# Performance work log

Hardware: AMD Instinct MI355X
Metric: run time of the kernel (lower is better)

## Reference

```python
import jax, jax.numpy as jnp
import numpy as np

N, S, C, G = 40000, 16, 96, 12
EPS = 1e-5

def ln(x, g, b):
    mu = jnp.mean(x, -1, keepdims=True)
    var = jnp.mean((x - mu) ** 2, -1, keepdims=True)
    return (x - mu) * jax.lax.rsqrt(var + EPS) * g + b

def setup_inputs() -> dict:
    key = jax.random.key(0)
    ks = jax.random.split(key, 20)
    s = 0.05
    inp = {
        'q': jax.random.normal(ks[0], (N, C), jnp.float32),
        'k': jax.random.normal(ks[1], (N, C), jnp.float32),
        'v': jax.random.normal(ks[2], (N, C), jnp.float32),
        'xyz': jax.random.normal(ks[3], (N, 3), jnp.float32),
        'reference_index': jax.random.randint(ks[4], (N, S), 0, N, jnp.int32),
        # linear_q: Linear(C,C)+LN(C)+ReLU
        'Wq': jax.random.normal(ks[5], (C, C), jnp.float32) * s,
        'bq': jnp.zeros((C,), jnp.float32),
        'gq': jnp.ones((C,), jnp.float32),
        'betaq': jnp.zeros((C,), jnp.float32),
        # linear_k
        'Wk': jax.random.normal(ks[6], (C, C), jnp.float32) * s,
        'bk': jnp.zeros((C,), jnp.float32),
        'gk': jnp.ones((C,), jnp.float32),
        'betak': jnp.zeros((C,), jnp.float32),
        # linear_v
        'Wv': jax.random.normal(ks[7], (C, C), jnp.float32) * s,
        'bv': jnp.zeros((C,), jnp.float32),
        # linear_p_bias: Linear(3,C)+LN(C)+ReLU+Linear(C,C)
        'Wp1': jax.random.normal(ks[8], (3, C), jnp.float32) * s,
        'bp1': jnp.zeros((C,), jnp.float32),
        'gp': jnp.ones((C,), jnp.float32),
        'betap': jnp.zeros((C,), jnp.float32),
        'Wp2': jax.random.normal(ks[9], (C, C), jnp.float32) * s,
        'bp2': jnp.zeros((C,), jnp.float32),
        # weight_encoding: Linear(C,G)+LN(G)+ReLU+Linear(G,G)
        'Ww1': jax.random.normal(ks[10], (C, G), jnp.float32) * s,
        'bw1': jnp.zeros((G,), jnp.float32),
        'gw': jnp.ones((G,), jnp.float32),
        'betaw': jnp.zeros((G,), jnp.float32),
        'Ww2': jax.random.normal(ks[11], (G, G), jnp.float32) * s,
        'bw2': jnp.zeros((G,), jnp.float32),
    }
    return inp

def reference(q, k, v, xyz, reference_index,
              Wq, bq, gq, betaq, Wk, bk, gk, betak, Wv, bv,
              Wp1, bp1, gp, betap, Wp2, bp2,
              Ww1, bw1, gw, betaw, Ww2, bw2):
    query = jax.nn.relu(ln(q @ Wq + bq, gq, betaq))            # [N, C]
    keyf  = jax.nn.relu(ln(k @ Wk + bk, gk, betak))            # [N, C]
    val   = v @ Wv + bv                                        # [N, C]

    idx = reference_index                                      # [N, S]
    mask = (idx >= 0).astype(q.dtype)                          # sign(idx+1)
    safe = jnp.clip(idx, 0, None)
    # pointops.grouping: gather w/ zero-fill at idx=-1; with_xyz prepends relative coords
    pos  = (xyz[safe] - xyz[:, None, :]) * mask[..., None]     # [N, S, 3]
    keyg = keyf[safe] * mask[..., None]                        # [N, S, C]
    valg = val[safe] * mask[..., None]                         # [N, S, C]

    rel = keyg - query[:, None, :]                             # [N, S, C]
    peb = jax.nn.relu(ln(pos @ Wp1 + bp1, gp, betap)) @ Wp2 + bp2
    rel = rel + peb
    valg = valg + peb

    w = jax.nn.relu(ln(rel @ Ww1 + bw1, gw, betaw)) @ Ww2 + bw2  # [N, S, G]
    w = jax.nn.softmax(w, axis=1) * mask[..., None]              # softmax over neighbors

    valg = valg.reshape(N, S, G, C // G)
    feat = jnp.einsum('nsgi,nsg->ngi', valg, w).reshape(N, C)
    return feat
```

## Files before the change

kernel.cpp:

```cpp
#include <hip/hip_runtime.h>

#define NN 40000
#define SS 16
#define CC 96
#define GG 12
#define CP 100

typedef __attribute__((ext_vector_type(8))) short bf16x8;
typedef __attribute__((ext_vector_type(4))) float f32x4;

__device__ __forceinline__ short f2bf(float f) {
    union { float f; unsigned u; } c; c.f = f;
    unsigned r = (c.u + 0x7fffu + ((c.u >> 16) & 1u)) >> 16;
    return (short)r;
}
__device__ __forceinline__ unsigned pack2bf(float hi, float lo) {
    unsigned a = __float_as_uint(hi) + 0x8000u;
    unsigned b = __float_as_uint(lo) + 0x8000u;
    return __builtin_amdgcn_perm(a, b, 0x07060302u);
}

template<int CTRL>
__device__ __forceinline__ float dppf(float x) {
    int r = __builtin_amdgcn_mov_dpp(__float_as_int(x), CTRL, 0xF, 0xF, true);
    return __int_as_float(r);
}
__device__ __forceinline__ float row16_sum(float x) {
    x += dppf<0xB1>(x);
    x += dppf<0x4E>(x);
    x += dppf<0x141>(x);
    x += dppf<0x140>(x);
    return x;
}
__device__ __forceinline__ float row16_max(float x) {
    x = fmaxf(x, dppf<0xB1>(x));
    x = fmaxf(x, dppf<0x4E>(x));
    x = fmaxf(x, dppf<0x141>(x));
    x = fmaxf(x, dppf<0x140>(x));
    return x;
}

#define J_W3   27648
#define J_P2   (J_W3 + 9216)
#define J_W1   (J_P2 + 1536)
#define J_WF   (J_W1 + 1536)
#define J_CF   (J_WF + 12)
#define J_S4   (J_CF + 4)
#define J_G    (J_S4 + 16)

__global__ void prep_kernel(const float* __restrict__ Wq, const float* __restrict__ Wk,
                            const float* __restrict__ Wv, const float* __restrict__ Wp2,
                            const float* __restrict__ Ww1, const float* __restrict__ bp2,
                            const float* __restrict__ bw1, const float* __restrict__ Wp1,
                            const float* __restrict__ bp1,
                            ushort* __restrict__ fragQKV, ushort* __restrict__ fragP2,
                            ushort* __restrict__ fragW1, ushort* __restrict__ fragWf,
                            float* __restrict__ cfused, float* __restrict__ stats)
{
    const int job = blockIdx.x*256 + threadIdx.x;
    if (job < J_W3) {
        const int which = job / 9216, o = job % 9216;
        const float* W = (which == 0) ? Wq : (which == 1) ? Wk : Wv;
        const int pos = o >> 3, j = o & 7;
        const int lane = pos & 63, ntkb = pos >> 6;
        const int nt = ntkb / 3, kb = ntkb - nt*3;
        const int col = nt*16 + (lane & 15), krow = kb*32 + (lane >> 4)*8 + j;
        fragQKV[job] = (ushort)f2bf(W[krow*CC + col]);
    } else if (job < J_P2) {
        const int o = job - J_W3;
        const int pos = o >> 3, j = o & 7;
        const int lane = pos & 63, ntkb = pos >> 6;
        const int nt = ntkb / 3, kb = ntkb - nt*3;
        const int col = nt*16 + (lane & 15), krow = kb*32 + (lane >> 4)*8 + j;
        fragP2[o] = (ushort)f2bf(Wp2[krow*CC + col]);
    } else if (job < J_W1) {
        const int o = job - J_P2;
        const int pos = o >> 3, j = o & 7;
        const int lane = pos & 63, kb = pos >> 6;
        const int col = lane & 15, krow = kb*32 + (lane >> 4)*8 + j;
        fragW1[o] = (col < GG) ? (ushort)f2bf(Ww1[krow*GG + col]) : (ushort)0;
    } else if (job < J_WF) {
        const int o = job - J_W1;
        const int pos = o >> 3, j = o & 7;
        const int lane = pos & 63, kb = pos >> 6;
        const int col = lane & 15, krow = kb*32 + (lane >> 4)*8 + j;
        float s = 0.f;
        if (col < GG) for (int jj = 0; jj < CC; ++jj) s += Wp2[krow*CC + jj] * Ww1[jj*GG + col];
        fragWf[o] = (col < GG) ? (ushort)f2bf(s) : (ushort)0;
    } else if (job < J_CF) {
        const int g = job - J_WF;
        float s = bw1[g];
        for (int jj = 0; jj < CC; ++jj) s += bp2[jj] * Ww1[jj*GG + g];
        cfused[g] = s;
    } else if (job < J_S4) {
        const int d = job - J_CF;
        float s = 0.f;
        for (int c = 0; c < CC; ++c) s += (d < 3) ? Wp1[d*CC + c] : bp1[c];
        stats[d] = s;
    } else if (job < J_G) {
        const int o = job - J_S4, d1 = o >> 2, d2 = o & 3;
        float s = 0.f;
        for (int c = 0; c < CC; ++c) {
            const float a1 = (d1 < 3) ? Wp1[d1*CC + c] : bp1[c];
            const float a2 = (d2 < 3) ? Wp1[d2*CC + c] : bp1[c];
            s += a1*a2;
        }
        stats[4 + o] = s;
    }
}

__global__ __launch_bounds__(256) void qkv_mfma(
    const float* __restrict__ q, const float* __restrict__ kx, const float* __restrict__ v,
    const float* __restrict__ bq, const float* __restrict__ gq, const float* __restrict__ betaq,
    const float* __restrict__ bk, const float* __restrict__ gk, const float* __restrict__ betak,
    const float* __restrict__ bv,
    const ushort* __restrict__ fragQKV, const ushort* __restrict__ fragW1,
    float* __restrict__ valout, float* __restrict__ qw1out, float* __restrict__ kw1out)
{
    __shared__ __align__(16) ushort sWf[9216];
    __shared__ float sbias[CC], sg[CC], sbeta[CC];
    __shared__ float sx[4][SS*CP];

    const int p = blockIdx.y;
    const float* X; const float* b;
    const float* g = nullptr; const float* beta = nullptr;
    if (p == 0)      { X = q;  b = bq; g = gq; beta = betaq; }
    else if (p == 1) { X = kx; b = bk; g = gk; beta = betak; }
    else             { X = v;  b = bv; }
    const bool has_ln = (p < 2);
    float* w1out = (p == 0) ? qw1out : kw1out;

    const int t = threadIdx.x;
    if (t < CC) {
        sbias[t] = b[t];
        if (has_ln) { sg[t] = g[t]; sbeta[t] = beta[t]; }
    }
    {
        const uint4* src = (const uint4*)(fragQKV + p*9216);
        for (int i = t; i < 1152; i += 256) ((uint4*)sWf)[i] = src[i];
    }

    const int lane = t & 63, w = t >> 6;
    const int c16 = lane & 15, quad = lane >> 4;

    bf16x8 Ww1f[3];
    if (has_ln) {
        #pragma unroll
        for (int kb = 0; kb < 3; ++kb) {
            union { bf16x8 v; uint4 u; } wu;
            wu.u = ((const uint4*)fragW1)[kb*64 + lane];
            Ww1f[kb] = wu.v;
        }
    }

    __syncthreads();

    const f32x4 zero4 = {0.f, 0.f, 0.f, 0.f};
    float* sxw = sx[w];
    const int tile = blockIdx.x*4 + w;
    const int row0 = tile * 16;

    const float* xr = X + (size_t)(row0 + c16)*CC;
    bf16x8 Af[3];
    #pragma unroll
    for (int kb = 0; kb < 3; ++kb) {
        const float4 a0 = *(const float4*)(xr + kb*32 + quad*8);
        const float4 a1 = *(const float4*)(xr + kb*32 + quad*8 + 4);
        union { bf16x8 v; uint u[4]; } au;
        au.u[0] = pack2bf(a0.y, a0.x);
        au.u[1] = pack2bf(a0.w, a0.z);
        au.u[2] = pack2bf(a1.y, a1.x);
        au.u[3] = pack2bf(a1.w, a1.z);
        Af[kb] = au.v;
    }

    f32x4 acc[6];
    #pragma unroll
    for (int nt = 0; nt < 6; ++nt) acc[nt] = zero4;
    #pragma unroll
    for (int kb = 0; kb < 3; ++kb)
        #pragma unroll
        for (int nt = 0; nt < 6; ++nt) {
            const bf16x8 bf = *(const bf16x8*)(sWf + ((nt*3 + kb)*64 + lane)*8);
            acc[nt] = __builtin_amdgcn_mfma_f32_16x16x32_bf16(Af[kb], bf, acc[nt], 0, 0, 0);
        }

    #pragma unroll
    for (int nt = 0; nt < 6; ++nt) {
        const float bb = sbias[nt*16 + c16];
        #pragma unroll
        for (int r = 0; r < 4; ++r) acc[nt][r] += bb;
    }

    if (has_ln) {
        #pragma unroll
        for (int r = 0; r < 4; ++r) {
            float sum = 0.f, sq = 0.f;
            #pragma unroll
            for (int nt = 0; nt < 6; ++nt) { float x = acc[nt][r]; sum += x; sq += x*x; }
            sum = row16_sum(sum); sq = row16_sum(sq);
            const float mu  = sum * (1.f/96.f);
            const float var = sq * (1.f/96.f) - mu*mu;
            const float rs  = rsqrtf(var + 1e-5f);
            #pragma unroll
            for (int nt = 0; nt < 6; ++nt) {
                const int c = nt*16 + c16;
                acc[nt][r] = fmaxf((acc[nt][r] - mu)*rs*sg[c] + sbeta[c], 0.f);
            }
        }
        #pragma unroll
        for (int nt = 0; nt < 6; ++nt)
            #pragma unroll
            for (int r = 0; r < 4; ++r)
                sxw[(quad*4 + r)*CP + nt*16 + c16] = acc[nt][r];

        bf16x8 aA[3];
        #pragma unroll
        for (int kb = 0; kb < 3; ++kb) {
            const float4 a0 = *(const float4*)(sxw + c16*CP + kb*32 + quad*8);
            const float4 a1 = *(const float4*)(sxw + c16*CP + kb*32 + quad*8 + 4);
            union { bf16x8 v; uint u[4]; } au;
            au.u[0] = pack2bf(a0.y, a0.x);
            au.u[1] = pack2bf(a0.w, a0.z);
            au.u[2] = pack2bf(a1.y, a1.x);
            au.u[3] = pack2bf(a1.w, a1.z);
            aA[kb] = au.v;
        }
        f32x4 o = zero4;
        #pragma unroll
        for (int kb = 0; kb < 3; ++kb)
            o = __builtin_amdgcn_mfma_f32_16x16x32_bf16(aA[kb], Ww1f[kb], o, 0, 0, 0);
        if (c16 < GG) {
            #pragma unroll
            for (int r = 0; r < 4; ++r)
                w1out[(size_t)(row0 + quad*4 + r)*GG + c16] = o[r];
        }
    } else {
        #pragma unroll
        for (int r = 0; r < 4; ++r)
            #pragma unroll
            for (int nt = 0; nt < 6; ++nt)
                valout[(size_t)(row0 + quad*4 + r)*CC + nt*16 + c16] = acc[nt][r];
    }
}

__global__ __launch_bounds__(256) void attn2(
    const float* __restrict__ xyz, const int* __restrict__ refidx,
    const float* __restrict__ gp,  const float* __restrict__ betap,
    const float* __restrict__ Wp1, const float* __restrict__ bp1,
    const float* __restrict__ bp2,
    const float* __restrict__ gw,  const float* __restrict__ betaw,
    const float* __restrict__ Ww2, const float* __restrict__ bw2,
    const float* __restrict__ cfused, const float* __restrict__ stats,
    const ushort* __restrict__ fragP2, const ushort* __restrict__ fragWf,
    const float* __restrict__ valw, const float* __restrict__ kw1w, const float* __restrict__ qw1w,
    float* __restrict__ out)
{
    __shared__ __align__(16) ushort sWp2f[9216];
    __shared__ __align__(16) ushort sWffl[1536];
    __shared__ float4 sA[CC];
    __shared__ float2 sGB[CC];
    __shared__ float  sbp2[CC];
    __shared__ float  sWw2[GG*GG];
    __shared__ float  sgw[16], sbetaw[16], sbw2[16], scf[16];
    __shared__ float  sstats[20];
    __shared__ float  ybv[4][SS*GG];
    __shared__ float  swv[4][SS*GG];

    const int t = threadIdx.x;
    if (t < CC) {
        sA[t]  = make_float4(Wp1[t], Wp1[CC + t], Wp1[2*CC + t], bp1[t]);
        sGB[t] = make_float2(gp[t], betap[t]);
        sbp2[t] = bp2[t];
    }
    if (t < GG*GG) sWw2[t] = Ww2[t];
    if (t < 16) {
        sgw[t]    = (t < GG) ? gw[t]     : 0.f;
        sbetaw[t] = (t < GG) ? betaw[t]  : 0.f;
        sbw2[t]   = (t < GG) ? bw2[t]    : 0.f;
        scf[t]    = (t < GG) ? cfused[t] : 0.f;
    }
    if (t < 20) sstats[t] = stats[t];
    for (int i = t; i < 1152; i += 256) ((uint4*)sWp2f)[i] = ((const uint4*)fragP2)[i];
    if (t < 192) ((uint4*)sWffl)[t] = ((const uint4*)fragWf)[t];

    const int lane = t & 63, w = t >> 6;
    const int c16 = lane & 15, quad = lane >> 4;
    const int gcl = (c16 < GG) ? c16 : (GG-1);

    __syncthreads();

    float* yb = ybv[w];
    float* sw = swv[w];
    const f32x4 zero4 = {0.f, 0.f, 0.f, 0.f};

    const int n = blockIdx.x*4 + w;

    const int   id   = refidx[(size_t)n*SS + c16];
    const float m    = (id >= 0) ? 1.f : 0.f;
    const int   safe = (id < 0) ? 0 : id;

    int sid[4]; float mr[4], kwv[4];
    #pragma unroll
    for (int r = 0; r < 4; ++r) {
        const int sd = refidx[(size_t)n*SS + quad*4 + r];
        mr[r]  = (sd >= 0) ? 1.f : 0.f;
        sid[r] = (sd < 0) ? 0 : sd;
    }
    #pragma unroll
    for (int r = 0; r < 4; ++r)
        kwv[r] = kw1w[(size_t)sid[r]*GG + gcl] * mr[r];
    const float qv = qw1w[(size_t)n*GG + gcl];

    const float px = (xyz[(size_t)safe*3 + 0] - xyz[(size_t)n*3 + 0]) * m;
    const float py = (xyz[(size_t)safe*3 + 1] - xyz[(size_t)n*3 + 1]) * m;
    const float pz = (xyz[(size_t)safe*3 + 2] - xyz[(size_t)n*3 + 2]) * m;

    const float mu = (px*sstats[0] + py*sstats[1] + pz*sstats[2] + sstats[3]) * (1.f/96.f);
    float e2 = 0.f;
    {
        const float p4[4] = {px, py, pz, 1.f};
        #pragma unroll
        for (int a = 0; a < 4; ++a) {
            float ta = 0.f;
            #pragma unroll
            for (int b2 = 0; b2 < 4; ++b2) ta = fmaf(sstats[4 + a*4 + b2], p4[b2], ta);
            e2 = fmaf(p4[a], ta, e2);
        }
    }
    const float var = e2*(1.f/96.f) - mu*mu;
    const float rs  = rsqrtf(var + 1e-5f);

    bf16x8 t1A[3];
    #pragma unroll
    for (int kb = 0; kb < 3; ++kb) {
        union { bf16x8 v; uint u[4]; } tu;
        #pragma unroll
        for (int jp = 0; jp < 4; ++jp) {
            float tt[2];
            #pragma unroll
            for (int h = 0; h < 2; ++h) {
                const int c = kb*32 + quad*8 + jp*2 + h;
                const float4 aw = sA[c];
                const float x = fmaf(px, aw.x, fmaf(py, aw.y, fmaf(pz, aw.z, aw.w)));
                const float2 gb = sGB[c];
                tt[h] = fmaxf(fmaf((x - mu)*rs, gb.x, gb.y), 0.f);
            }
            tu.u[jp] = pack2bf(tt[1], tt[0]);
        }
        t1A[kb] = tu.v;
    }

    f32x4 t2 = zero4;
    #pragma unroll
    for (int kb = 0; kb < 3; ++kb) {
        const bf16x8 wf = *(const bf16x8*)(sWffl + (kb*64 + lane)*8);
        t2 = __builtin_amdgcn_mfma_f32_16x16x32_bf16(t1A[kb], wf, t2, 0, 0, 0);
    }
    #pragma unroll
    for (int r = 0; r < 4; ++r)
        t2[r] += kwv[r] - qv + scf[c16];

    #pragma unroll
    for (int r = 0; r < 4; ++r) {
        const float x = (c16 < GG) ? t2[r] : 0.f;
        const float s1 = row16_sum(x);
        const float s2 = row16_sum(x*x);
        const float mu2  = s1 * (1.f/12.f);
        const float var2 = s2 * (1.f/12.f) - mu2*mu2;
        const float rs2  = rsqrtf(var2 + 1e-5f);
        const float y    = fmaxf((t2[r] - mu2)*rs2*sgw[c16] + sbetaw[c16], 0.f);
        if (c16 < GG) yb[(quad*4 + r)*GG + c16] = y;
    }

    float w3[3];
    #pragma unroll
    for (int gi = 0; gi < 3; ++gi) {
        const int gpp = quad + gi*4;
        float a2 = sbw2[gpp];
        #pragma unroll
        for (int gg2 = 0; gg2 < GG; ++gg2)
            a2 += yb[c16*GG + gg2] * sWw2[gg2*GG + gpp];
        w3[gi] = a2;
    }

    #pragma unroll
    for (int gi = 0; gi < 3; ++gi) {
        const float mx = row16_max(w3[gi]);
        const float e  = __expf(w3[gi] - mx);
        const float tot = row16_sum(e);
        w3[gi] = e / tot * m;
    }
    #pragma unroll
    for (int gi = 0; gi < 3; ++gi)
        sw[c16*GG + quad + 4*gi] = w3[gi];

    #pragma unroll
    for (int ntp = 0; ntp < 3; ++ntp) {
        const int nt0 = 2*ntp, nt1 = 2*ntp + 1;
        float va[2][4];
        #pragma unroll
        for (int h = 0; h < 2; ++h)
            #pragma unroll
            for (int r = 0; r < 4; ++r)
                va[h][r] = valw[(size_t)sid[r]*CC + (2*ntp + h)*16 + c16];

        f32x4 pa = zero4, pb = zero4;
        #pragma unroll
        for (int kb = 0; kb < 3; ++kb) {
            const bf16x8 bfa = *(const bf16x8*)(sWp2f + ((nt0*3 + kb)*64 + lane)*8);
            const bf16x8 bfb = *(const bf16x8*)(sWp2f + ((nt1*3 + kb)*64 + lane)*8);
            pa = __builtin_amdgcn_mfma_f32_16x16x32_bf16(t1A[kb], bfa, pa, 0, 0, 0);
            pb = __builtin_amdgcn_mfma_f32_16x16x32_bf16(t1A[kb], bfb, pb, 0, 0, 0);
        }
        #pragma unroll
        for (int h = 0; h < 2; ++h) {
            const int nt = 2*ntp + h;
            const f32x4& pc = (h == 0) ? pa : pb;
            const float b2   = sbp2[nt*16 + c16];
            const int   gidx = 2*nt + (c16 >> 3);
            float a2 = 0.f;
            #pragma unroll
            for (int r = 0; r < 4; ++r)
                a2 += (pc[r] + b2 + mr[r]*va[h][r]) * sw[(quad*4 + r)*GG + gidx];
            a2 += __shfl_xor(a2, 16, 64);
            a2 += __shfl_xor(a2, 32, 64);
            if (quad == 0) out[(size_t)n*CC + nt*16 + c16] = a2;
        }
    }
}

extern "C" void kernel_launch(void* const* d_in, const int* in_sizes, int n_in,
                              void* d_out, int out_size, void* d_ws, size_t ws_size,
                              hipStream_t stream)
{
    const float* q     = (const float*)d_in[0];
    const float* k     = (const float*)d_in[1];
    const float* v     = (const float*)d_in[2];
    const float* xyz   = (const float*)d_in[3];
    const int*   ridx  = (const int*)d_in[4];
    const float* Wq    = (const float*)d_in[5];
    const float* bq    = (const float*)d_in[6];
    const float* gq    = (const float*)d_in[7];
    const float* betaq = (const float*)d_in[8];
    const float* Wk    = (const float*)d_in[9];
    const float* bk    = (const float*)d_in[10];
    const float* gk    = (const float*)d_in[11];
    const float* betak = (const float*)d_in[12];
    const float* Wv    = (const float*)d_in[13];
    const float* bv    = (const float*)d_in[14];
    const float* Wp1   = (const float*)d_in[15];
    const float* bp1   = (const float*)d_in[16];
    const float* gp    = (const float*)d_in[17];
    const float* betap = (const float*)d_in[18];
    const float* Wp2   = (const float*)d_in[19];
    const float* bp2   = (const float*)d_in[20];
    const float* Ww1   = (const float*)d_in[21];
    const float* bw1   = (const float*)d_in[22];
    const float* gw    = (const float*)d_in[23];
    const float* betaw = (const float*)d_in[24];
    const float* Ww2   = (const float*)d_in[25];
    const float* bw2   = (const float*)d_in[26];
    float* out = (float*)d_out;

    float* ws = (float*)d_ws;
    float* valw   = ws;
    float* kw1w   = valw + (size_t)NN*CC;
    float* qw1w   = kw1w + (size_t)NN*GG;
    float* cfused = qw1w + (size_t)NN*GG;
    float* statsp = cfused + 16;
    ushort* fragQKV = (ushort*)(statsp + 24);
    ushort* fragP2  = fragQKV + 3*9216;
    ushort* fragW1  = fragP2 + 9216;
    ushort* fragWf  = fragW1 + 1536;

    prep_kernel<<<dim3(157, 1, 1), 256, 0, stream>>>(
        Wq, Wk, Wv, Wp2, Ww1, bp2, bw1, Wp1, bp1,
        fragQKV, fragP2, fragW1, fragWf, cfused, statsp);

    qkv_mfma<<<dim3(625, 3, 1), 256, 0, stream>>>(
        q, k, v, bq, gq, betaq, bk, gk, betak, bv,
        fragQKV, fragW1, valw, qw1w, kw1w);

    attn2<<<dim3(10000, 1, 1), 256, 0, stream>>>(
        xyz, ridx, gp, betap, Wp1, bp1, bp2,
        gw, betaw, Ww2, bw2, cfused, statsp,
        fragP2, fragWf, valw, kw1w, qw1w, out);
}
```

Before: 223.2 us.

## Read MFMA weight fragments from global/registers instead of staging in LDS

Both kernels stop copying the bf16 weight fragments into shared memory for every block. The MFMA B operands are now read directly from global memory, which is cached, or held in registers for the small Wf fragment. In qkv_mfma the LayerNorm output is staged in LDS as bf16 rather than fp32, so the MFMA A operand loads as one vector with no repacking. In attn2 the two per-wave scratch buffers are merged into one. Together these cut per-block setup work and LDS footprint, aiming for higher occupancy. The cost is extra global/L2 traffic on the inner MFMA loop, and the merged buffer relies on in-wave ordering of LDS accesses for correctness.

Measured after the change: 234.3 us. +5.0%, slower.

```diff
diff --git a/kernel.cpp b/kernel.cpp
--- a/kernel.cpp
+++ b/kernel.cpp
@@ -5,6 +5,7 @@
 #define CC 96
 #define GG 12
 #define CP 100
+#define SXP 104
 
 typedef __attribute__((ext_vector_type(8))) short bf16x8;
 typedef __attribute__((ext_vector_type(4))) float f32x4;
@@ -18,6 +19,9 @@
     unsigned a = __float_as_uint(hi) + 0x8000u;
     unsigned b = __float_as_uint(lo) + 0x8000u;
     return __builtin_amdgcn_perm(a, b, 0x07060302u);
+}
+__device__ __forceinline__ ushort f2bf_hu(float f) {
+    return (ushort)((__float_as_uint(f) + 0x8000u) >> 16);
 }
 
 template<int CTRL>
@@ -117,9 +121,8 @@
     const ushort* __restrict__ fragQKV, const ushort* __restrict__ fragW1,
     float* __restrict__ valout, float* __restrict__ qw1out, float* __restrict__ kw1out)
 {
-    __shared__ __align__(16) ushort sWf[9216];
     __shared__ float sbias[CC], sg[CC], sbeta[CC];
-    __shared__ float sx[4][SS*CP];
+    __shared__ __align__(16) ushort sx2[4][16*SXP];
 
     const int p = blockIdx.y;
     const float* X; const float* b;
@@ -135,13 +138,10 @@
         sbias[t] = b[t];
         if (has_ln) { sg[t] = g[t]; sbeta[t] = beta[t]; }
     }
-    {
-        const uint4* src = (const uint4*)(fragQKV + p*9216);
-        for (int i = t; i < 1152; i += 256) ((uint4*)sWf)[i] = src[i];
-    }
 
     const int lane = t & 63, w = t >> 6;
     const int c16 = lane & 15, quad = lane >> 4;
+    const ushort* fragW = fragQKV + p*9216;
 
     bf16x8 Ww1f[3];
     if (has_ln) {
@@ -156,7 +156,7 @@
     __syncthreads();
 
     const f32x4 zero4 = {0.f, 0.f, 0.f, 0.f};
-    float* sxw = sx[w];
+    ushort* sxw = sx2[w];
     const int tile = blockIdx.x*4 + w;
     const int row0 = tile * 16;
 
@@ -181,7 +181,7 @@
     for (int kb = 0; kb < 3; ++kb)
         #pragma unroll
         for (int nt = 0; nt < 6; ++nt) {
-            const bf16x8 bf = *(const bf16x8*)(sWf + ((nt*3 + kb)*64 + lane)*8);
+            const bf16x8 bf = *(const bf16x8*)(fragW + ((nt*3 + kb)*64 + lane)*8);
             acc[nt] = __builtin_amdgcn_mfma_f32_16x16x32_bf16(Af[kb], bf, acc[nt], 0, 0, 0);
         }
 
@@ -212,24 +212,14 @@
         for (int nt = 0; nt < 6; ++nt)
             #pragma unroll
             for (int r = 0; r < 4; ++r)
-                sxw[(quad*4 + r)*CP + nt*16 + c16] = acc[nt][r];
-
-        bf16x8 aA[3];
+                sxw[(quad*4 + r)*SXP + nt*16 + c16] = f2bf_hu(acc[nt][r]);
+
+        f32x4 o = zero4;
         #pragma unroll
         for (int kb = 0; kb < 3; ++kb) {
-            const float4 a0 = *(const float4*)(sxw + c16*CP + kb*32 + quad*8);
-            const float4 a1 = *(const float4*)(sxw + c16*CP + kb*32 + quad*8 + 4);
-            union { bf16x8 v; uint u[4]; } au;
-            au.u[0] = pack2bf(a0.y, a0.x);
-            au.u[1] = pack2bf(a0.w, a0.z);
-            au.u[2] = pack2bf(a1.y, a1.x);
-            au.u[3] = pack2bf(a1.w, a1.z);
-            aA[kb] = au.v;
-        }
-        f32x4 o = zero4;
-        #pragma unroll
-        for (int kb = 0; kb < 3; ++kb)
-            o = __builtin_amdgcn_mfma_f32_16x16x32_bf16(aA[kb], Ww1f[kb], o, 0, 0, 0);
+            const bf16x8 aA = *(const bf16x8*)(sxw + c16*SXP + kb*32 + quad*8);
+            o = __builtin_amdgcn_mfma_f32_16x16x32_bf16(aA, Ww1f[kb], o, 0, 0, 0);
+        }
         if (c16 < GG) {
             #pragma unroll
             for (int r = 0; r < 4; ++r)
@@ -256,16 +246,13 @@
     const float* __restrict__ valw, const float* __restrict__ kw1w, const float* __restrict__ qw1w,
     float* __restrict__ out)
 {
-    __shared__ __align__(16) ushort sWp2f[9216];
-    __shared__ __align__(16) ushort sWffl[1536];
     __shared__ float4 sA[CC];
     __shared__ float2 sGB[CC];
     __shared__ float  sbp2[CC];
     __shared__ float  sWw2[GG*GG];
     __shared__ float  sgw[16], sbetaw[16], sbw2[16], scf[16];
     __shared__ float  sstats[20];
-    __shared__ float  ybv[4][SS*GG];
-    __shared__ float  swv[4][SS*GG];
+    __shared__ float  ybuf[4][SS*GG];
 
     const int t = threadIdx.x;
     if (t < CC) {
@@ -281,17 +268,23 @@
         scf[t]    = (t < GG) ? cfused[t] : 0.f;
     }
     if (t < 20) sstats[t] = stats[t];
-    for (int i = t; i < 1152; i += 256) ((uint4*)sWp2f)[i] = ((const uint4*)fragP2)[i];
-    if (t < 192) ((uint4*)sWffl)[t] = ((const uint4*)fragWf)[t];
 
     const int lane = t & 63, w = t >> 6;
     const int c16 = lane & 15, quad = lane >> 4;
     const int gcl = (c16 < GG) ? c16 : (GG-1);
 
+    bf16x8 Wff[3];
+    #pragma unroll
+    for (int kb = 0; kb < 3; ++kb) {
+        union { bf16x8 v; uint4 u; } wu;
+        wu.u = ((const uint4*)fragWf)[kb*64 + lane];
+        Wff[kb] = wu.v;
+    }
+
     __syncthreads();
 
-    float* yb = ybv[w];
-    float* sw = swv[w];
+    float* yb = ybuf[w];
+    float* sw = ybuf[w];
     const f32x4 zero4 = {0.f, 0.f, 0.f, 0.f};
 
     const int n = blockIdx.x*4 + w;
@@ -353,10 +346,8 @@
 
     f32x4 t2 = zero4;
     #pragma unroll
-    for (int kb = 0; kb < 3; ++kb) {
-        const bf16x8 wf = *(const bf16x8*)(sWffl + (kb*64 + lane)*8);
-        t2 = __builtin_amdgcn_mfma_f32_16x16x32_bf16(t1A[kb], wf, t2, 0, 0, 0);
-    }
+    for (int kb = 0; kb < 3; ++kb)
+        t2 = __builtin_amdgcn_mfma_f32_16x16x32_bf16(t1A[kb], Wff[kb], t2, 0, 0, 0);
     #pragma unroll
     for (int r = 0; r < 4; ++r)
         t2[r] += kwv[r] - qv + scf[c16];
@@ -408,8 +399,8 @@
         f32x4 pa = zero4, pb = zero4;
         #pragma unroll
         for (int kb = 0; kb < 3; ++kb) {
-            const bf16x8 bfa = *(const bf16x8*)(sWp2f + ((nt0*3 + kb)*64 + lane)*8);
-            const bf16x8 bfb = *(const bf16x8*)(sWp2f + ((nt1*3 + kb)*64 + lane)*8);
+            const bf16x8 bfa = *(const bf16x8*)(fragP2 + ((nt0*3 + kb)*64 + lane)*8);
+            const bf16x8 bfb = *(const bf16x8*)(fragP2 + ((nt1*3 + kb)*64 + lane)*8);
             pa = __builtin_amdgcn_mfma_f32_16x16x32_bf16(t1A[kb], bfa, pa, 0, 0, 0);
             pb = __builtin_amdgcn_mfma_f32_16x16x32_bf16(t1A[kb], bfb, pb, 0, 0, 0);
         }
```
